# Performance work log

Hardware: AMD Instinct MI355X
Metric: run time of the kernel (lower is better)

Reference implementation:

```python
import jax, jax.numpy as jnp
import numpy as np

N_NODES = 50000
N_EDGES = 800000
IN_CH = 64
HID = 128
LAST_HID = 256


def setup_inputs() -> dict:
    key = jax.random.key(0)
    ks = jax.random.split(key, 12)
    x = jax.random.normal(ks[0], (N_NODES, IN_CH), dtype=jnp.float32)
    edge_index = jax.random.randint(ks[1], (2, N_EDGES), 0, N_NODES, dtype=jnp.int64)
    s = lambda fan_in: 1.0 / np.sqrt(fan_in)
    return {
        "x": x,
        "edge_index": edge_index,
        # SAGEConv1: lin_l (aggregated neighbors, with bias), lin_r (root, no bias)
        "W1l": jax.random.normal(ks[2], (HID, IN_CH), dtype=jnp.float32) * s(IN_CH),
        "b1l": jnp.zeros((HID,), dtype=jnp.float32),
        "W1r": jax.random.normal(ks[3], (HID, IN_CH), dtype=jnp.float32) * s(IN_CH),
        # SAGEConv2 -> 1 channel
        "W2l": jax.random.normal(ks[4], (1, HID), dtype=jnp.float32) * s(HID),
        "b2l": jnp.zeros((1,), dtype=jnp.float32),
        "W2r": jax.random.normal(ks[5], (1, HID), dtype=jnp.float32) * s(HID),
        # fc1 (LazyLinear bound to N_NODES input features) and fc2
        "fc1_W": jax.random.normal(ks[6], (LAST_HID, N_NODES), dtype=jnp.float32) * s(N_NODES),
        "fc1_b": jnp.zeros((LAST_HID,), dtype=jnp.float32),
        "fc2_W": jax.random.normal(ks[7], (1, LAST_HID), dtype=jnp.float32) * s(LAST_HID),
        "fc2_b": jnp.zeros((1,), dtype=jnp.float32),
    }


def _sage_conv(h, src, dst, Wl, bl, Wr, n_nodes):
    # PyG SAGEConv (mean aggr): out = lin_l(mean_{j in N(i)} x_j) + lin_r(x_i)
    msgs = h[src]  # [E, F] gather of source node features
    summed = jax.ops.segment_sum(msgs, dst, num_segments=n_nodes)  # [N, F]
    deg = jax.ops.segment_sum(jnp.ones((src.shape[0],), h.dtype), dst, num_segments=n_nodes)
    agg = summed / jnp.maximum(deg, 1.0)[:, None]
    return agg @ Wl.T + bl + h @ Wr.T


def reference(x, edge_index, W1l, b1l, W1r, W2l, b2l, W2r, fc1_W, fc1_b, fc2_W, fc2_b):
    n = x.shape[0]
    src, dst = edge_index[0], edge_index[1]
    h = jax.nn.relu(_sage_conv(x, src, dst, W1l, b1l, W1r, n))   # [N, HID]
    h = jax.nn.relu(_sage_conv(h, src, dst, W2l, b2l, W2r, n))   # [N, 1]
    v = h[:, 0]                                                   # [N]
    z = fc1_W @ v + fc1_b                                         # [LAST_HID]
    pred = fc2_W @ z + fc2_b                                      # [1]
    return pred[0]  # scalar (torch.squeeze)
```

## Files before the change

### kernel.cpp

```cpp
#include <hip/hip_runtime.h>

#define N_NODESC 50000
#define N_EDGESC 800000
#define MAXDEG 64

typedef short bf16x8 __attribute__((ext_vector_type(8)));
typedef float f32x4  __attribute__((ext_vector_type(4)));

__device__ inline unsigned short f2bf(float f) {
    unsigned u = __float_as_uint(f);
    unsigned r = u + 0x7FFFu + ((u >> 16) & 1u);
    return (unsigned short)(r >> 16);
}
__device__ inline float bf2f(unsigned short h) {
    return __uint_as_float(((unsigned)h) << 16);
}

__global__ void k0_init(int* __restrict__ deg, float* __restrict__ z) {
    int i = blockIdx.x * 256 + threadIdx.x;
    if (i < N_NODESC) deg[i] = 0;
    if (i < 256) z[i] = 0.0f;
}

#define K1_BLOCKS 2048
#define K1_EPB (N_EDGESC / (K1_BLOCKS / 8))
__global__ void k1_bucket(const int* __restrict__ ei, int* __restrict__ deg,
                          int* __restrict__ bucket) {
    int g   = blockIdx.x & 7;
    int idx = blockIdx.x >> 3;
    int lo = g * (N_NODESC / 8), hi = lo + (N_NODESC / 8);
    int e0 = idx * K1_EPB;
    for (int i = threadIdx.x; i < K1_EPB; i += 256) {
        int e = e0 + i;
        int dst = ei[N_EDGESC + e];
        int src = ei[e];
        if (dst >= lo && dst < hi) {
            int slot = atomicAdd(&deg[dst], 1);
            if (slot < MAXDEG) bucket[dst * MAXDEG + slot] = src;
        }
    }
}

__global__ void k2_agg(const float* __restrict__ x, const int* __restrict__ deg,
                       const int* __restrict__ bucket, float* __restrict__ agg) {
    int lane = threadIdx.x & 63;
    int node = blockIdx.x * 4 + (threadIdx.x >> 6);
    int g  = lane >> 4;
    int c4 = lane & 15;
    int d = deg[node];
    int c = min(d, MAXDEG);
    int bidx = bucket[node * MAXDEG + lane];
    float4 acc = make_float4(0.f, 0.f, 0.f, 0.f);
    for (int k = 0; k < c; k += 8) {
        int i0 = k + g, i1 = k + 4 + g;
        int b0 = __shfl(bidx, i0);
        int b1 = __shfl(bidx, i1);
        if (i0 < c) {
            float4 v = ((const float4*)(x + b0 * 64))[c4];
            acc.x += v.x; acc.y += v.y; acc.z += v.z; acc.w += v.w;
        }
        if (i1 < c) {
            float4 v = ((const float4*)(x + b1 * 64))[c4];
            acc.x += v.x; acc.y += v.y; acc.z += v.z; acc.w += v.w;
        }
    }
    #pragma unroll
    for (int m = 16; m <= 32; m <<= 1) {
        acc.x += __shfl_xor(acc.x, m);
        acc.y += __shfl_xor(acc.y, m);
        acc.z += __shfl_xor(acc.z, m);
        acc.w += __shfl_xor(acc.w, m);
    }
    if (g == 0) {
        float inv = 1.0f / (float)max(d, 1);
        ((float4*)(agg + node * 64))[c4] =
            make_float4(acc.x * inv, acc.y * inv, acc.z * inv, acc.w * inv);
    }
}

#define K3S 144

__launch_bounds__(256, 3)
__global__ void k3_mm_mfma(const float* __restrict__ x, const float* __restrict__ agg,
                           const float* __restrict__ W1l, const float* __restrict__ b1l,
                           const float* __restrict__ W1r,
                           const float* __restrict__ W2l, const float* __restrict__ W2r,
                           float* __restrict__ s_out, float* __restrict__ t_out) {
    __shared__ __align__(16) short sAhi[64 * K3S];
    __shared__ __align__(16) short sAlo[64 * K3S];
    __shared__ float sS[64], sT[64];

    int tid = threadIdx.x;
    int lane = tid & 63;
    int wave = tid >> 6;
    int col = lane & 15;
    int quad = lane >> 4;
    int node0 = blockIdx.x * 64;

    if (tid < 64) { sS[tid] = 0.f; sT[tid] = 0.f; }

    int o_base = wave * 32;
    bf16x8 bhi[2][4], blo[2][4];
    float bias_r[2], w2l_r[2], w2r_r[2];
    #pragma unroll
    for (int oc = 0; oc < 2; oc++) {
        int o = o_base + oc * 16 + col;
        bias_r[oc] = b1l[o]; w2l_r[oc] = W2l[o]; w2r_r[oc] = W2r[o];
        #pragma unroll
        for (int ks = 0; ks < 4; ks++) {
            int k0 = ks * 32 + quad * 8;
            const float* wrow = (k0 < 64) ? (W1r + o * 64 + k0)
                                          : (W1l + o * 64 + (k0 - 64));
            #pragma unroll
            for (int j = 0; j < 8; j++) {
                float w = wrow[j];
                unsigned short h = f2bf(w);
                bhi[oc][ks][j] = (short)h;
                blo[oc][ks][j] = (short)f2bf(w - bf2f(h));
            }
        }
    }

    #pragma unroll
    for (int i = 0; i < 4; i++) {
        int c = tid + 256 * i;
        int n = c >> 4, kc = c & 15;
        int node = node0 + n;
        float v[8];
        if (node < N_NODESC) {
            const float* src = (kc < 8) ? (x + node * 64 + kc * 8)
                                        : (agg + node * 64 + (kc - 8) * 8);
            float4 v0 = *(const float4*)src;
            float4 v1 = *(const float4*)(src + 4);
            v[0] = v0.x; v[1] = v0.y; v[2] = v0.z; v[3] = v0.w;
            v[4] = v1.x; v[5] = v1.y; v[6] = v1.z; v[7] = v1.w;
        } else {
            #pragma unroll
            for (int j = 0; j < 8; j++) v[j] = 0.f;
        }
        bf16x8 hv, lv;
        #pragma unroll
        for (int j = 0; j < 8; j++) {
            unsigned short h = f2bf(v[j]);
            hv[j] = (short)h;
            lv[j] = (short)f2bf(v[j] - bf2f(h));
        }
        *(bf16x8*)&sAhi[n * K3S + kc * 8] = hv;
        *(bf16x8*)&sAlo[n * K3S + kc * 8] = lv;
    }
    __syncthreads();

    f32x4 acc[4][2];
    #pragma unroll
    for (int nt = 0; nt < 4; nt++)
        #pragma unroll
        for (int oc = 0; oc < 2; oc++) acc[nt][oc] = (f32x4)0.f;

    #pragma unroll
    for (int ks = 0; ks < 4; ks++) {
        #pragma unroll
        for (int nt = 0; nt < 4; nt++) {
            int off = (nt * 16 + col) * K3S + ks * 32 + quad * 8;
            bf16x8 ah = *(const bf16x8*)&sAhi[off];
            bf16x8 al = *(const bf16x8*)&sAlo[off];
            #pragma unroll
            for (int oc = 0; oc < 2; oc++) {
                acc[nt][oc] = __builtin_amdgcn_mfma_f32_16x16x32_bf16(ah, bhi[oc][ks], acc[nt][oc], 0, 0, 0);
                acc[nt][oc] = __builtin_amdgcn_mfma_f32_16x16x32_bf16(al, bhi[oc][ks], acc[nt][oc], 0, 0, 0);
                acc[nt][oc] = __builtin_amdgcn_mfma_f32_16x16x32_bf16(ah, blo[oc][ks], acc[nt][oc], 0, 0, 0);
            }
        }
    }

    #pragma unroll
    for (int nt = 0; nt < 4; nt++) {
        float sp[4] = {0.f, 0.f, 0.f, 0.f};
        float tp[4] = {0.f, 0.f, 0.f, 0.f};
        #pragma unroll
        for (int oc = 0; oc < 2; oc++)
            #pragma unroll
            for (int reg = 0; reg < 4; reg++) {
                float h = fmaxf(acc[nt][oc][reg] + bias_r[oc], 0.f);
                sp[reg] += h * w2l_r[oc];
                tp[reg] += h * w2r_r[oc];
            }
        #pragma unroll
        for (int reg = 0; reg < 4; reg++) {
            #pragma unroll
            for (int m = 1; m <= 8; m <<= 1) {
                sp[reg] += __shfl_xor(sp[reg], m);
                tp[reg] += __shfl_xor(tp[reg], m);
            }
        }
        if (col == 0) {
            int nn = nt * 16 + quad * 4;
            #pragma unroll
            for (int reg = 0; reg < 4; reg++) {
                atomicAdd(&sS[nn + reg], sp[reg]);
                atomicAdd(&sT[nn + reg], tp[reg]);
            }
        }
    }
    __syncthreads();
    if (tid < 64) {
        int node = node0 + tid;
        if (node < N_NODESC) { s_out[node] = sS[tid]; t_out[node] = sT[tid]; }
    }
}

__global__ void k4_layer2(const float* __restrict__ s, const float* __restrict__ t,
                          const int* __restrict__ deg, const int* __restrict__ bucket,
                          const float* __restrict__ b2l, float* __restrict__ v) {
    int tid = threadIdx.x;
    int lane = tid & 15;
    int node = blockIdx.x * 16 + (tid >> 4);
    int d = deg[node];
    int c = min(d, MAXDEG);
    float sum = 0.f;
    for (int k = lane; k < c; k += 16) sum += s[bucket[node * MAXDEG + k]];
    sum += __shfl_xor(sum, 1);
    sum += __shfl_xor(sum, 2);
    sum += __shfl_xor(sum, 4);
    sum += __shfl_xor(sum, 8);
    if (lane == 0) {
        float h = sum / (float)max(d, 1) + b2l[0] + t[node];
        v[node] = fmaxf(h, 0.f);
    }
}

__global__ void k5_fc1(const float* __restrict__ fc1W, const float* __restrict__ v,
                       float* __restrict__ z) {
    int row = blockIdx.x >> 2;
    int part = blockIdx.x & 3;
    const float4* W4 = (const float4*)(fc1W + row * 50000 + part * 12500);
    const float4* v4 = (const float4*)(v + part * 12500);
    float sum = 0.f;
    for (int i = threadIdx.x; i < 3125; i += 256) {
        float4 w = W4[i], a = v4[i];
        sum += w.x * a.x + w.y * a.y + w.z * a.z + w.w * a.w;
    }
    #pragma unroll
    for (int m = 1; m < 64; m <<= 1) sum += __shfl_xor(sum, m);
    __shared__ float red[4];
    if ((threadIdx.x & 63) == 0) red[threadIdx.x >> 6] = sum;
    __syncthreads();
    if (threadIdx.x == 0) atomicAdd(&z[row], red[0] + red[1] + red[2] + red[3]);
}

__global__ void k6_head(const float* __restrict__ z, const float* __restrict__ fc1b,
                        const float* __restrict__ fc2W, const float* __restrict__ fc2b,
                        float* __restrict__ out) {
    int t = threadIdx.x;
    float val = (z[t] + fc1b[t]) * fc2W[t];
    #pragma unroll
    for (int m = 1; m < 64; m <<= 1) val += __shfl_xor(val, m);
    __shared__ float red[4];
    if ((t & 63) == 0) red[t >> 6] = val;
    __syncthreads();
    if (t == 0) out[0] = red[0] + red[1] + red[2] + red[3] + fc2b[0];
}

extern "C" void kernel_launch(void* const* d_in, const int* in_sizes, int n_in,
                              void* d_out, int out_size, void* d_ws, size_t ws_size,
                              hipStream_t stream) {
    const float* x    = (const float*)d_in[0];
    const int*   ei   = (const int*)d_in[1];
    const float* W1l  = (const float*)d_in[2];
    const float* b1l  = (const float*)d_in[3];
    const float* W1r  = (const float*)d_in[4];
    const float* W2l  = (const float*)d_in[5];
    const float* b2l  = (const float*)d_in[6];
    const float* W2r  = (const float*)d_in[7];
    const float* fc1W = (const float*)d_in[8];
    const float* fc1b = (const float*)d_in[9];
    const float* fc2W = (const float*)d_in[10];
    const float* fc2b = (const float*)d_in[11];
    float* out = (float*)d_out;

    char* ws = (char*)d_ws;
    int*   deg    = (int*)  (ws + 0);
    float* z      = (float*)(ws + 200192);
    int*   bucket = (int*)  (ws + 201216);
    float* agg    = (float*)(ws + 13001216);
    float* s      = (float*)(ws + 25801216);
    float* t      = (float*)(ws + 26001216);
    float* v      = (float*)(ws + 26201216);

    k0_init   <<<196,   256, 0, stream>>>(deg, z);
    k1_bucket <<<K1_BLOCKS, 256, 0, stream>>>(ei, deg, bucket);
    k2_agg    <<<12500, 256, 0, stream>>>(x, deg, bucket, agg);
    k3_mm_mfma<<<782,  256, 0, stream>>>(x, agg, W1l, b1l, W1r, W2l, W2r, s, t);
    k4_layer2 <<<3125,  256, 0, stream>>>(s, t, deg, bucket, b2l, v);
    k5_fc1    <<<1024,  256, 0, stream>>>(fc1W, v, z);
    k6_head   <<<1,     256, 0, stream>>>(z, fc1b, fc2W, fc2b, out);
}
```

Baseline: 213.1 us.

## Prepack W1 into bf16 hi/lo fragments once and drop shared atomics

Adds a small kernel that converts W1l/W1r into split bf16 hi/lo fragments laid out for the MFMA B operand. The matmul kernel then loads those fragments directly instead of having every block reload and convert the fp32 weights. The activation loads for x and agg are issued before the weight loads so their latency overlaps. The per-wave shared-memory atomicAdds are replaced by per-wave partial arrays that are summed at the end. This costs one extra kernel launch and a small amount of workspace.

Result: no change. 210.2 us (-1.4%).

```diff
diff --git a/kernel.cpp b/kernel.cpp
--- a/kernel.cpp
+++ b/kernel.cpp
@@ -20,6 +20,33 @@
     int i = blockIdx.x * 256 + threadIdx.x;
     if (i < N_NODESC) deg[i] = 0;
     if (i < 256) z[i] = 0.0f;
+}
+
+__global__ void kW_pack(const float* __restrict__ W1l, const float* __restrict__ W1r,
+                        short* __restrict__ pkhi, short* __restrict__ pklo) {
+    int ks = blockIdx.x;
+    int t  = threadIdx.x;
+    int o  = t & 127;
+    int h  = t >> 7;
+    const float* src = (ks < 2) ? (W1r + o * 64 + ks * 32)
+                                : (W1l + o * 64 + (ks - 2) * 32);
+    #pragma unroll
+    for (int qi = 0; qi < 2; qi++) {
+        int q = 2 * h + qi;
+        float4 a = *(const float4*)(src + q * 8);
+        float4 b = *(const float4*)(src + q * 8 + 4);
+        float v[8] = {a.x, a.y, a.z, a.w, b.x, b.y, b.z, b.w};
+        bf16x8 hv, lv;
+        #pragma unroll
+        for (int j = 0; j < 8; j++) {
+            unsigned short hh = f2bf(v[j]);
+            hv[j] = (short)hh;
+            lv[j] = (short)f2bf(v[j] - bf2f(hh));
+        }
+        int idx = ((ks * 4 + q) * 128 + o) * 8;
+        *(bf16x8*)&pkhi[idx] = hv;
+        *(bf16x8*)&pklo[idx] = lv;
+    }
 }
 
 #define K1_BLOCKS 2048
@@ -82,13 +109,13 @@
 
 __launch_bounds__(256, 3)
 __global__ void k3_mm_mfma(const float* __restrict__ x, const float* __restrict__ agg,
-                           const float* __restrict__ W1l, const float* __restrict__ b1l,
-                           const float* __restrict__ W1r,
+                           const short* __restrict__ pkhi, const short* __restrict__ pklo,
+                           const float* __restrict__ b1l,
                            const float* __restrict__ W2l, const float* __restrict__ W2r,
                            float* __restrict__ s_out, float* __restrict__ t_out) {
     __shared__ __align__(16) short sAhi[64 * K3S];
     __shared__ __align__(16) short sAlo[64 * K3S];
-    __shared__ float sS[64], sT[64];
+    __shared__ float sSp[4][64], sTp[4][64];
 
     int tid = threadIdx.x;
     int lane = tid & 63;
@@ -97,47 +124,44 @@
     int quad = lane >> 4;
     int node0 = blockIdx.x * 64;
 
-    if (tid < 64) { sS[tid] = 0.f; sT[tid] = 0.f; }
-
-    int o_base = wave * 32;
-    bf16x8 bhi[2][4], blo[2][4];
-    float bias_r[2], w2l_r[2], w2r_r[2];
-    #pragma unroll
-    for (int oc = 0; oc < 2; oc++) {
-        int o = o_base + oc * 16 + col;
-        bias_r[oc] = b1l[o]; w2l_r[oc] = W2l[o]; w2r_r[oc] = W2r[o];
-        #pragma unroll
-        for (int ks = 0; ks < 4; ks++) {
-            int k0 = ks * 32 + quad * 8;
-            const float* wrow = (k0 < 64) ? (W1r + o * 64 + k0)
-                                          : (W1l + o * 64 + (k0 - 64));
-            #pragma unroll
-            for (int j = 0; j < 8; j++) {
-                float w = wrow[j];
-                unsigned short h = f2bf(w);
-                bhi[oc][ks][j] = (short)h;
-                blo[oc][ks][j] = (short)f2bf(w - bf2f(h));
-            }
-        }
-    }
-
+    float4 sv0[4], sv1[4];
     #pragma unroll
     for (int i = 0; i < 4; i++) {
         int c = tid + 256 * i;
         int n = c >> 4, kc = c & 15;
         int node = node0 + n;
-        float v[8];
         if (node < N_NODESC) {
             const float* src = (kc < 8) ? (x + node * 64 + kc * 8)
                                         : (agg + node * 64 + (kc - 8) * 8);
-            float4 v0 = *(const float4*)src;
-            float4 v1 = *(const float4*)(src + 4);
-            v[0] = v0.x; v[1] = v0.y; v[2] = v0.z; v[3] = v0.w;
-            v[4] = v1.x; v[5] = v1.y; v[6] = v1.z; v[7] = v1.w;
+            sv0[i] = *(const float4*)src;
+            sv1[i] = *(const float4*)(src + 4);
         } else {
-            #pragma unroll
-            for (int j = 0; j < 8; j++) v[j] = 0.f;
-        }
+            sv0[i] = make_float4(0.f, 0.f, 0.f, 0.f);
+            sv1[i] = make_float4(0.f, 0.f, 0.f, 0.f);
+        }
+    }
+
+    int o_base = wave * 32;
+    bf16x8 bhi[2][4], blo[2][4];
+    float bias_r[2], w2l_r[2], w2r_r[2];
+    #pragma unroll
+    for (int oc = 0; oc < 2; oc++) {
+        int o = o_base + oc * 16 + col;
+        bias_r[oc] = b1l[o]; w2l_r[oc] = W2l[o]; w2r_r[oc] = W2r[o];
+        #pragma unroll
+        for (int ks = 0; ks < 4; ks++) {
+            int idx = ((ks * 4 + quad) * 128 + o) * 8;
+            bhi[oc][ks] = *(const bf16x8*)&pkhi[idx];
+            blo[oc][ks] = *(const bf16x8*)&pklo[idx];
+        }
+    }
+
+    #pragma unroll
+    for (int i = 0; i < 4; i++) {
+        int c = tid + 256 * i;
+        int n = c >> 4, kc = c & 15;
+        float v[8] = {sv0[i].x, sv0[i].y, sv0[i].z, sv0[i].w,
+                      sv1[i].x, sv1[i].y, sv1[i].z, sv1[i].w};
         bf16x8 hv, lv;
         #pragma unroll
         for (int j = 0; j < 8; j++) {
@@ -196,15 +220,18 @@
             int nn = nt * 16 + quad * 4;
             #pragma unroll
             for (int reg = 0; reg < 4; reg++) {
-                atomicAdd(&sS[nn + reg], sp[reg]);
-                atomicAdd(&sT[nn + reg], tp[reg]);
+                sSp[wave][nn + reg] = sp[reg];
+                sTp[wave][nn + reg] = tp[reg];
             }
         }
     }
     __syncthreads();
     if (tid < 64) {
         int node = node0 + tid;
-        if (node < N_NODESC) { s_out[node] = sS[tid]; t_out[node] = sT[tid]; }
+        if (node < N_NODESC) {
+            s_out[node] = sSp[0][tid] + sSp[1][tid] + sSp[2][tid] + sSp[3][tid];
+            t_out[node] = sTp[0][tid] + sTp[1][tid] + sTp[2][tid] + sTp[3][tid];
+        }
     }
 }
 
@@ -285,11 +312,14 @@
     float* s      = (float*)(ws + 25801216);
     float* t      = (float*)(ws + 26001216);
     float* v      = (float*)(ws + 26201216);
+    short* pkhi   = (short*)(ws + 26401280);
+    short* pklo   = (short*)(ws + 26434048);
 
     k0_init   <<<196,   256, 0, stream>>>(deg, z);
+    kW_pack   <<<4,     256, 0, stream>>>(W1l, W1r, pkhi, pklo);
     k1_bucket <<<K1_BLOCKS, 256, 0, stream>>>(ei, deg, bucket);
     k2_agg    <<<12500, 256, 0, stream>>>(x, deg, bucket, agg);
-    k3_mm_mfma<<<782,  256, 0, stream>>>(x, agg, W1l, b1l, W1r, W2l, W2r, s, t);
+    k3_mm_mfma<<<782,  256, 0, stream>>>(x, agg, pkhi, pklo, b1l, W2l, W2r, s, t);
     k4_layer2 <<<3125,  256, 0, stream>>>(s, t, deg, bucket, b2l, v);
     k5_fc1    <<<1024,  256, 0, stream>>>(fc1W, v, z);
     k6_head   <<<1,     256, 0, stream>>>(z, fc1b, fc2W, fc2b, out);
```
